# Performance work log

Hardware: AMD Instinct MI355X
Metric: run time of the kernel (lower is better)

The kernel has to match this reference:

```python
import jax, jax.numpy as jnp
import numpy as np

B, S, D, H = 1, 2048, 768, 12
WIN = 128            # window_size
HALF = WIN // 2      # 64
WN = WIN + 1         # each position attends to [i-64, i+64] inclusive -> 129 keys
DH = D // H


def setup_inputs() -> dict:
    key = jax.random.key(0)
    ks = jax.random.split(key, 8)
    scale = 0.02
    return {
        "query": jax.random.normal(ks[0], (B, S, D), dtype=jnp.float32),
        "key":   jax.random.normal(ks[1], (B, S, D), dtype=jnp.float32),
        "value": jax.random.normal(ks[2], (B, S, D), dtype=jnp.float32),
        "Wq": jax.random.normal(ks[3], (D, D), dtype=jnp.float32) * scale,
        "bq": jnp.zeros((D,), dtype=jnp.float32),
        "Wk": jax.random.normal(ks[4], (D, D), dtype=jnp.float32) * scale,
        "bk": jnp.zeros((D,), dtype=jnp.float32),
        "Wv": jax.random.normal(ks[5], (D, D), dtype=jnp.float32) * scale,
        "bv": jnp.zeros((D,), dtype=jnp.float32),
        "Wo": jax.random.normal(ks[6], (D, D), dtype=jnp.float32) * scale,
        "bo": jnp.zeros((D,), dtype=jnp.float32),
    }


def reference(query, key, value, Wq, bq, Wk, bk, Wv, bv, Wo, bo):
    b, s, d = query.shape
    # Linear projections, split heads: [B,S,H,DH]
    q = (query @ Wq + bq).reshape(b, s, H, DH)
    k = (key   @ Wk + bk).reshape(b, s, H, DH)
    v = (value @ Wv + bv).reshape(b, s, H, DH)

    # Window gather indices: pos[i, j] = i - HALF + j, j in [0, WN)
    pos = jnp.arange(s)[:, None] + (jnp.arange(WN)[None, :] - HALF)  # [S, WN]
    valid = (pos >= 0) & (pos < s)                                   # [S, WN]
    idx = jnp.clip(pos, 0, s - 1)

    kw = k[:, idx]  # [B, S, WN, H, DH]
    vw = v[:, idx]  # [B, S, WN, H, DH]

    scores = jnp.einsum('bshd,bswhd->bhsw', q, kw) / np.sqrt(DH)     # [B,H,S,WN]
    scores = jnp.where(valid[None, None, :, :], scores, -jnp.inf)
    attn = jax.nn.softmax(scores, axis=-1)

    ctx = jnp.einsum('bhsw,bswhd->bshd', attn, vw).reshape(b, s, d)  # [B,S,D]
    return ctx @ Wo + bo
```

## Files before the change

### kernel.cpp

```cpp
#include <hip/hip_runtime.h>
#include <math.h>

#define S_LEN 2048
#define DM 768
#define NHEAD 12
#define DHEAD 64
#define HALF_W 64

typedef _Float16 half8 __attribute__((ext_vector_type(8)));
typedef _Float16 half4_t __attribute__((ext_vector_type(4)));
typedef float floatx4 __attribute__((ext_vector_type(4)));

typedef const __attribute__((address_space(1))) unsigned int* gas_ptr;
typedef __attribute__((address_space(3))) unsigned int* las_ptr;
__device__ __forceinline__ void gld_lds16(const void* g, void* l) {
  __builtin_amdgcn_global_load_lds((gas_ptr)g, (las_ptr)l, 16, 0, 0);
}

__global__ __launch_bounds__(256)
void prep_w_kernel(const float* __restrict__ Wq, const float* __restrict__ Wk,
                   const float* __restrict__ Wv, const float* __restrict__ Wo,
                   _Float16* __restrict__ Tq, _Float16* __restrict__ Tk,
                   _Float16* __restrict__ Tv, _Float16* __restrict__ To) {
  __shared__ float t[64][65];
  int b = blockIdx.x;
  int z = b / 144, rem = b % 144;
  const float* W = z == 0 ? Wq : z == 1 ? Wk : z == 2 ? Wv : Wo;
  _Float16* T = z == 0 ? Tq : z == 1 ? Tk : z == 2 ? Tv : To;
  int n0 = (rem % 12) * 64, k0 = (rem / 12) * 64;
  int tx = threadIdx.x & 15, ty = threadIdx.x >> 4;
#pragma unroll
  for (int i = 0; i < 4; ++i) {
    int row = ty + i * 16;
    float4 v = *(const float4*)(W + (size_t)(k0 + row) * DM + n0 + tx * 4);
    t[row][tx * 4 + 0] = v.x; t[row][tx * 4 + 1] = v.y;
    t[row][tx * 4 + 2] = v.z; t[row][tx * 4 + 3] = v.w;
  }
  __syncthreads();
#pragma unroll
  for (int i = 0; i < 4; ++i) {
    int nn = ty + i * 16, kk = tx * 4;
    half4_t h = {(_Float16)t[kk + 0][nn], (_Float16)t[kk + 1][nn],
                 (_Float16)t[kk + 2][nn], (_Float16)t[kk + 3][nn]};
    *(half4_t*)(T + (size_t)(n0 + nn) * DM + k0 + kk) = h;
  }
}

#define GBM 64
#define GBN 128
#define GBK 64
#define ACH 17

__global__ __launch_bounds__(256, 4)
void gemm_qkv_kernel(const float* __restrict__ A0, const float* __restrict__ A1,
                     const float* __restrict__ A2, const _Float16* __restrict__ W0,
                     const _Float16* __restrict__ W1, const _Float16* __restrict__ W2,
                     const float* __restrict__ b0, const float* __restrict__ b1,
                     const float* __restrict__ b2, _Float16* __restrict__ Q,
                     _Float16* __restrict__ K, _Float16* __restrict__ Vt) {
  __shared__ __align__(16) float Asf[GBM * ACH * 4];
  __shared__ __align__(16) _Float16 Bs[GBN * GBK];
  const int bid = blockIdx.x;
  const int xcd = bid & 7;
  const int li = bid >> 3;
  const int panel = xcd * 12 + li / 6;
  const int nb = li % 6;
  const int z = panel >> 5;
  const int m0 = (panel & 31) * GBM;
  const int n0 = nb * GBN;
  const float* A = z == 0 ? A0 : z == 1 ? A1 : A2;
  const _Float16* Wt = z == 0 ? W0 : z == 1 ? W1 : W2;
  const float* bias = z == 0 ? b0 : z == 1 ? b1 : b2;

  const int tid = threadIdx.x;
  const int lane = tid & 63;
  const int w = tid >> 6;
  const int lr = lane & 15;
  const int lq = lane >> 4;
  const int wm = w >> 1, wn = w & 1;
  const int wb = tid & 192;

  floatx4 acc[2][4] = {};

  for (int k0 = 0; k0 < DM; k0 += GBK) {
    __syncthreads();
#pragma unroll
    for (int i = 0; i < 5; ++i) {
      if (i < 4 || tid < 64) {
        int s = i * 256 + tid;
        int m = s / ACH, pos = s % ACH;
        int ch = pos < 16 ? pos : 15;
        gld_lds16(A + (size_t)(m0 + m) * DM + k0 + ch * 4, &Asf[(i * 256 + wb) * 4]);
      }
    }
#pragma unroll
    for (int i = 0; i < 4; ++i) {
      int c = i * 256 + tid;
      int n = c >> 3, j = c & 7, jg = j ^ (n & 7);
      gld_lds16(Wt + (size_t)(n0 + n) * DM + k0 + jg * 8, &Bs[(i * 256 + wb) * 8]);
    }
    __syncthreads();

#pragma unroll
    for (int kh = 0; kh < 2; ++kh) {
      half8 af[2], bf[4];
#pragma unroll
      for (int mt = 0; mt < 2; ++mt) {
        int m = wm * 32 + mt * 16 + lr;
        int j0 = kh * 8 + lq * 2;
        float4 f0 = *(const float4*)&Asf[(m * ACH + j0) * 4];
        float4 f1 = *(const float4*)&Asf[(m * ACH + j0 + 1) * 4];
        af[mt] = half8{(_Float16)f0.x, (_Float16)f0.y, (_Float16)f0.z, (_Float16)f0.w,
                       (_Float16)f1.x, (_Float16)f1.y, (_Float16)f1.z, (_Float16)f1.w};
      }
#pragma unroll
      for (int nt = 0; nt < 4; ++nt) {
        int n = wn * 64 + nt * 16 + lr;
        int j = (kh * 4 + lq) ^ (n & 7);
        bf[nt] = *(const half8*)&Bs[n * GBK + j * 8];
      }
#pragma unroll
      for (int mt = 0; mt < 2; ++mt)
#pragma unroll
        for (int nt = 0; nt < 4; ++nt)
          acc[mt][nt] = __builtin_amdgcn_mfma_f32_16x16x32_f16(af[mt], bf[nt], acc[mt][nt], 0, 0, 0);
    }
  }

#pragma unroll
  for (int mt = 0; mt < 2; ++mt) {
    int row0 = m0 + wm * 32 + mt * 16 + lq * 4;
#pragma unroll
    for (int nt = 0; nt < 4; ++nt) {
      int col = n0 + wn * 64 + nt * 16 + lr;
      float bv = bias[col];
      if (z == 2) {
        half4_t o = {(_Float16)(acc[mt][nt][0] + bv), (_Float16)(acc[mt][nt][1] + bv),
                     (_Float16)(acc[mt][nt][2] + bv), (_Float16)(acc[mt][nt][3] + bv)};
        *(half4_t*)(Vt + (size_t)col * S_LEN + row0) = o;
      } else {
        _Float16* H = z == 0 ? Q : K;
#pragma unroll
        for (int rr = 0; rr < 4; ++rr)
          H[(size_t)(row0 + rr) * DM + col] = (_Float16)(acc[mt][nt][rr] + bv);
      }
    }
  }
}

#define OBM 64
#define OBN 64

__global__ __launch_bounds__(256, 6)
void gemm_out_kernel(const _Float16* __restrict__ A, const _Float16* __restrict__ Wt,
                     const float* __restrict__ bias, float* __restrict__ C) {
  __shared__ __align__(16) _Float16 As[OBM * GBK];
  __shared__ __align__(16) _Float16 Bs[OBN * GBK];
  const int bid = blockIdx.x;
  const int xcd = bid & 7;
  const int li = bid >> 3;
  const int m0 = (xcd * 4 + li / 12) * OBM;
  const int n0 = (li % 12) * OBN;
  const int tid = threadIdx.x;
  const int lane = tid & 63;
  const int w = tid >> 6;
  const int lr = lane & 15;
  const int lq = lane >> 4;
  const int wm = w >> 1, wn = w & 1;
  const int wb = tid & 192;

  floatx4 acc[2][2] = {};

  for (int k0 = 0; k0 < DM; k0 += GBK) {
    __syncthreads();
#pragma unroll
    for (int i = 0; i < 2; ++i) {
      int c = i * 256 + tid;
      int m = c >> 3, j = c & 7, jg = j ^ (m & 7);
      gld_lds16(A + (size_t)(m0 + m) * DM + k0 + jg * 8, &As[(i * 256 + wb) * 8]);
    }
#pragma unroll
    for (int i = 0; i < 2; ++i) {
      int c = i * 256 + tid;
      int n = c >> 3, j = c & 7, jg = j ^ (n & 7);
      gld_lds16(Wt + (size_t)(n0 + n) * DM + k0 + jg * 8, &Bs[(i * 256 + wb) * 8]);
    }
    __syncthreads();

#pragma unroll
    for (int kh = 0; kh < 2; ++kh) {
      half8 af[2], bf[2];
#pragma unroll
      for (int mt = 0; mt < 2; ++mt) {
        int m = wm * 32 + mt * 16 + lr;
        int j = (kh * 4 + lq) ^ (m & 7);
        af[mt] = *(const half8*)&As[m * GBK + j * 8];
      }
#pragma unroll
      for (int nt = 0; nt < 2; ++nt) {
        int n = wn * 32 + nt * 16 + lr;
        int j = (kh * 4 + lq) ^ (n & 7);
        bf[nt] = *(const half8*)&Bs[n * GBK + j * 8];
      }
#pragma unroll
      for (int mt = 0; mt < 2; ++mt)
#pragma unroll
        for (int nt = 0; nt < 2; ++nt)
          acc[mt][nt] = __builtin_amdgcn_mfma_f32_16x16x32_f16(af[mt], bf[nt], acc[mt][nt], 0, 0, 0);
    }
  }

#pragma unroll
  for (int mt = 0; mt < 2; ++mt) {
    int row0 = m0 + wm * 32 + mt * 16 + lq * 4;
#pragma unroll
    for (int nt = 0; nt < 2; ++nt) {
      int col = n0 + wn * 32 + nt * 16 + lr;
      float bv = bias[col];
#pragma unroll
      for (int rr = 0; rr < 4; ++rr)
        C[(size_t)(row0 + rr) * DM + col] = acc[mt][nt][rr] + bv;
    }
  }
}

#define ATQ 32

__global__ __launch_bounds__(256, 3)
void swattn_mfma_kernel(const _Float16* __restrict__ qh, const _Float16* __restrict__ kh,
                        const _Float16* __restrict__ vt, _Float16* __restrict__ ctx) {
  __shared__ __align__(16) _Float16 Ks[160 * 64];
  __shared__ __align__(16) _Float16 Vs[64 * 168];
  __shared__ __align__(16) _Float16 QP[32 * 168];
  __shared__ float red[4][32];

  const int tid = threadIdx.x;
  const int lane = tid & 63, w = tid >> 6;
  const int lr = lane & 15, lq = lane >> 4;
  const int bid = blockIdx.x;
  const int x = bid & 7, mid = (bid >> 3) & 7, h = bid >> 6;
  const int s0 = (x * 8 + mid) * ATQ;
  const int wb = tid & 192;

  {
    int r = tid >> 3, j = tid & 7, jg = j ^ (r & 7);
    gld_lds16(qh + (size_t)(s0 + r) * DM + h * DHEAD + jg * 8, &QP[wb * 8]);
  }
#pragma unroll
  for (int i = 0; i < 5; ++i) {
    int c = i * 256 + tid;
    int r = c >> 3, j = c & 7, jg = j ^ (r & 7);
    int pos = s0 - HALF_W + r;
    pos = pos < 0 ? 0 : (pos > S_LEN - 1 ? S_LEN - 1 : pos);
    gld_lds16(kh + (size_t)pos * DM + h * DHEAD + jg * 8, &Ks[(i * 256 + wb) * 8]);
  }
#pragma unroll
  for (int i = 0; i < 6; ++i) {
    int c = i * 256 + tid;
    if (c < 1344) {
      int r = c / 21, j = c % 21;
      int cb = s0 - HALF_W + j * 8;
      cb = cb < 0 ? 0 : (cb > S_LEN - 8 ? S_LEN - 8 : cb);
      gld_lds16(vt + (size_t)(h * DHEAD + r) * S_LEN + cb, &Vs[(i * 256 + wb) * 8]);
    }
  }
  __syncthreads();

  const int qt = w & 1, ph = w >> 1;
  floatx4 sc[5];
  {
    half8 aq[2];
#pragma unroll
    for (int k2 = 0; k2 < 2; ++k2) {
      int r = qt * 16 + lr, j = (k2 * 4 + lq) ^ (r & 7);
      aq[k2] = *(const half8*)&QP[r * DHEAD + j * 8];
    }
#pragma unroll
    for (int t = 0; t < 5; ++t) {
      int pt = ph * 5 + t;
      floatx4 a = {};
#pragma unroll
      for (int k2 = 0; k2 < 2; ++k2) {
        int r = pt * 16 + lr, j = (k2 * 4 + lq) ^ (r & 7);
        half8 bk = *(const half8*)&Ks[r * DHEAD + j * 8];
        a = __builtin_amdgcn_mfma_f32_16x16x32_f16(aq[k2], bk, a, 0, 0, 0);
      }
      sc[t] = a;
    }
  }

  const int qbase = qt * 16 + lq * 4;
  float m4[4] = {-1e30f, -1e30f, -1e30f, -1e30f};
#pragma unroll
  for (int t = 0; t < 5; ++t) {
    int p = (ph * 5 + t) * 16 + lr;
    int g = s0 - HALF_W + p;
#pragma unroll
    for (int rr = 0; rr < 4; ++rr) {
      int q = qbase + rr;
      bool ok = (p >= q) && (p <= q + 128) && (g >= 0) && (g < S_LEN);
      float v = ok ? sc[t][rr] * 0.125f : -1e30f;
      sc[t][rr] = v;
      m4[rr] = fmaxf(m4[rr], v);
    }
  }
#pragma unroll
  for (int off = 1; off <= 8; off <<= 1)
#pragma unroll
    for (int rr = 0; rr < 4; ++rr) m4[rr] = fmaxf(m4[rr], __shfl_xor(m4[rr], off, 64));
  if (lr == 0)
#pragma unroll
    for (int rr = 0; rr < 4; ++rr) red[ph][qbase + rr] = m4[rr];
  __syncthreads();

  float ss[4] = {0.f, 0.f, 0.f, 0.f};
  float mm[4];
#pragma unroll
  for (int rr = 0; rr < 4; ++rr)
    mm[rr] = fmaxf(red[0][qbase + rr], red[1][qbase + rr]);
#pragma unroll
  for (int t = 0; t < 5; ++t)
#pragma unroll
    for (int rr = 0; rr < 4; ++rr) {
      float e = __expf(sc[t][rr] - mm[rr]);
      sc[t][rr] = e;
      ss[rr] += e;
    }
#pragma unroll
  for (int off = 1; off <= 8; off <<= 1)
#pragma unroll
    for (int rr = 0; rr < 4; ++rr) ss[rr] += __shfl_xor(ss[rr], off, 64);
  if (lr == 0)
#pragma unroll
    for (int rr = 0; rr < 4; ++rr) red[2 + ph][qbase + rr] = ss[rr];
  __syncthreads();

#pragma unroll
  for (int rr = 0; rr < 4; ++rr) {
    float inv = 1.f / (red[2][qbase + rr] + red[3][qbase + rr]);
#pragma unroll
    for (int t = 0; t < 5; ++t) {
      int p = (ph * 5 + t) * 16 + lr;
      QP[(qbase + rr) * 168 + p] = (_Float16)(sc[t][rr] * inv);
    }
  }
  __syncthreads();

  {
    const int qt2 = w & 1;
    const int dt0 = (w >> 1) * 2;
    floatx4 a0 = {}, a1 = {};
#pragma unroll
    for (int ks = 0; ks < 5; ++ks) {
      half8 ap = *(const half8*)&QP[(qt2 * 16 + lr) * 168 + ks * 32 + lq * 8];
      half8 bv0 = *(const half8*)&Vs[(dt0 * 16 + lr) * 168 + ks * 32 + lq * 8];
      half8 bv1 = *(const half8*)&Vs[((dt0 + 1) * 16 + lr) * 168 + ks * 32 + lq * 8];
      a0 = __builtin_amdgcn_mfma_f32_16x16x32_f16(ap, bv0, a0, 0, 0, 0);
      a1 = __builtin_amdgcn_mfma_f32_16x16x32_f16(ap, bv1, a1, 0, 0, 0);
    }
#pragma unroll
    for (int rr = 0; rr < 4; ++rr) {
      size_t row = (size_t)(s0 + qt2 * 16 + lq * 4 + rr) * DM + h * DHEAD;
      ctx[row + dt0 * 16 + lr] = (_Float16)a0[rr];
      ctx[row + (dt0 + 1) * 16 + lr] = (_Float16)a1[rr];
    }
  }
}

extern "C" void kernel_launch(void* const* d_in, const int* in_sizes, int n_in,
                              void* d_out, int out_size, void* d_ws, size_t ws_size,
                              hipStream_t stream) {
  const float* query = (const float*)d_in[0];
  const float* key   = (const float*)d_in[1];
  const float* value = (const float*)d_in[2];
  const float* Wq = (const float*)d_in[3];
  const float* bq = (const float*)d_in[4];
  const float* Wk = (const float*)d_in[5];
  const float* bk = (const float*)d_in[6];
  const float* Wv = (const float*)d_in[7];
  const float* bv = (const float*)d_in[8];
  const float* Wo = (const float*)d_in[9];
  const float* bo = (const float*)d_in[10];
  float* out = (float*)d_out;

  const size_t nel = (size_t)S_LEN * DM;
  const size_t wel = (size_t)DM * DM;
  _Float16* Wtq = (_Float16*)d_ws;
  _Float16* Wtk = Wtq + wel;
  _Float16* Wtv = Wtk + wel;
  _Float16* Wto = Wtv + wel;
  _Float16* qh = Wto + wel;
  _Float16* khb = qh + nel;
  _Float16* Vtg = khb + nel;
  _Float16* ctxh = Vtg + nel;

  prep_w_kernel<<<dim3(576), 256, 0, stream>>>(Wq, Wk, Wv, Wo, Wtq, Wtk, Wtv, Wto);
  gemm_qkv_kernel<<<dim3(576), 256, 0, stream>>>(
      query, key, value, Wtq, Wtk, Wtv, bq, bk, bv, qh, khb, Vtg);
  swattn_mfma_kernel<<<dim3((S_LEN / ATQ) * NHEAD), 256, 0, stream>>>(qh, khb, Vtg, ctxh);
  gemm_out_kernel<<<dim3(384), 256, 0, stream>>>(ctxh, Wto, bo, out);
}
```

Baseline: 130.1 us.

## Pre-convert QKV activations to fp16 in prep kernel and simplify GEMM A tiles

The prep kernel now also converts the query/key/value activations from fp32 to fp16 into workspace buffers, so the QKV GEMM loads fp16 A tiles with an XOR-swizzled layout and does no per-fragment conversion. LDS use for A is halved, which allows raising the occupancy hint in launch bounds from 4 to 6. The cost is an extra full read and write pass over the activations in the prep kernel. The ctx buffer reuses the now-dead Aq workspace region.

```diff
diff --git a/kernel.cpp b/kernel.cpp
--- a/kernel.cpp
+++ b/kernel.cpp
@@ -18,47 +18,60 @@
 }
 
 __global__ __launch_bounds__(256)
-void prep_w_kernel(const float* __restrict__ Wq, const float* __restrict__ Wk,
-                   const float* __restrict__ Wv, const float* __restrict__ Wo,
-                   _Float16* __restrict__ Tq, _Float16* __restrict__ Tk,
-                   _Float16* __restrict__ Tv, _Float16* __restrict__ To) {
+void prep_kernel(const float* __restrict__ Wq, const float* __restrict__ Wk,
+                 const float* __restrict__ Wv, const float* __restrict__ Wo,
+                 _Float16* __restrict__ Tq, _Float16* __restrict__ Tk,
+                 _Float16* __restrict__ Tv, _Float16* __restrict__ To,
+                 const float* __restrict__ qs, const float* __restrict__ ks,
+                 const float* __restrict__ vs, _Float16* __restrict__ Aq,
+                 _Float16* __restrict__ Ak, _Float16* __restrict__ Av) {
   __shared__ float t[64][65];
   int b = blockIdx.x;
-  int z = b / 144, rem = b % 144;
-  const float* W = z == 0 ? Wq : z == 1 ? Wk : z == 2 ? Wv : Wo;
-  _Float16* T = z == 0 ? Tq : z == 1 ? Tk : z == 2 ? Tv : To;
-  int n0 = (rem % 12) * 64, k0 = (rem / 12) * 64;
-  int tx = threadIdx.x & 15, ty = threadIdx.x >> 4;
-#pragma unroll
-  for (int i = 0; i < 4; ++i) {
-    int row = ty + i * 16;
-    float4 v = *(const float4*)(W + (size_t)(k0 + row) * DM + n0 + tx * 4);
-    t[row][tx * 4 + 0] = v.x; t[row][tx * 4 + 1] = v.y;
-    t[row][tx * 4 + 2] = v.z; t[row][tx * 4 + 3] = v.w;
-  }
-  __syncthreads();
-#pragma unroll
-  for (int i = 0; i < 4; ++i) {
-    int nn = ty + i * 16, kk = tx * 4;
-    half4_t h = {(_Float16)t[kk + 0][nn], (_Float16)t[kk + 1][nn],
-                 (_Float16)t[kk + 2][nn], (_Float16)t[kk + 3][nn]};
-    *(half4_t*)(T + (size_t)(n0 + nn) * DM + k0 + kk) = h;
+  if (b < 576) {
+    int z = b / 144, rem = b % 144;
+    const float* W = z == 0 ? Wq : z == 1 ? Wk : z == 2 ? Wv : Wo;
+    _Float16* T = z == 0 ? Tq : z == 1 ? Tk : z == 2 ? Tv : To;
+    int n0 = (rem % 12) * 64, k0 = (rem / 12) * 64;
+    int tx = threadIdx.x & 15, ty = threadIdx.x >> 4;
+#pragma unroll
+    for (int i = 0; i < 4; ++i) {
+      int row = ty + i * 16;
+      float4 v = *(const float4*)(W + (size_t)(k0 + row) * DM + n0 + tx * 4);
+      t[row][tx * 4 + 0] = v.x; t[row][tx * 4 + 1] = v.y;
+      t[row][tx * 4 + 2] = v.z; t[row][tx * 4 + 3] = v.w;
+    }
+    __syncthreads();
+#pragma unroll
+    for (int i = 0; i < 4; ++i) {
+      int nn = ty + i * 16, kk = tx * 4;
+      half4_t h = {(_Float16)t[kk + 0][nn], (_Float16)t[kk + 1][nn],
+                   (_Float16)t[kk + 2][nn], (_Float16)t[kk + 3][nn]};
+      *(half4_t*)(T + (size_t)(n0 + nn) * DM + k0 + kk) = h;
+    }
+  } else {
+    int i = b - 576;
+    int z = i / 1536;
+    const float* s = z == 0 ? qs : z == 1 ? ks : vs;
+    _Float16* d = z == 0 ? Aq : z == 1 ? Ak : Av;
+    int idx = (i % 1536) * 256 + threadIdx.x;
+    float4 v = ((const float4*)s)[idx];
+    half4_t h = {(_Float16)v.x, (_Float16)v.y, (_Float16)v.z, (_Float16)v.w};
+    ((half4_t*)d)[idx] = h;
   }
 }
 
 #define GBM 64
 #define GBN 128
 #define GBK 64
-#define ACH 17
-
-__global__ __launch_bounds__(256, 4)
-void gemm_qkv_kernel(const float* __restrict__ A0, const float* __restrict__ A1,
-                     const float* __restrict__ A2, const _Float16* __restrict__ W0,
+
+__global__ __launch_bounds__(256, 6)
+void gemm_qkv_kernel(const _Float16* __restrict__ A0, const _Float16* __restrict__ A1,
+                     const _Float16* __restrict__ A2, const _Float16* __restrict__ W0,
                      const _Float16* __restrict__ W1, const _Float16* __restrict__ W2,
                      const float* __restrict__ b0, const float* __restrict__ b1,
                      const float* __restrict__ b2, _Float16* __restrict__ Q,
                      _Float16* __restrict__ K, _Float16* __restrict__ Vt) {
-  __shared__ __align__(16) float Asf[GBM * ACH * 4];
+  __shared__ __align__(16) _Float16 As[GBM * GBK];
   __shared__ __align__(16) _Float16 Bs[GBN * GBK];
   const int bid = blockIdx.x;
   const int xcd = bid & 7;
@@ -68,7 +81,7 @@
   const int z = panel >> 5;
   const int m0 = (panel & 31) * GBM;
   const int n0 = nb * GBN;
-  const float* A = z == 0 ? A0 : z == 1 ? A1 : A2;
+  const _Float16* A = z == 0 ? A0 : z == 1 ? A1 : A2;
   const _Float16* Wt = z == 0 ? W0 : z == 1 ? W1 : W2;
   const float* bias = z == 0 ? b0 : z == 1 ? b1 : b2;
 
@@ -85,13 +98,10 @@
   for (int k0 = 0; k0 < DM; k0 += GBK) {
     __syncthreads();
 #pragma unroll
-    for (int i = 0; i < 5; ++i) {
-      if (i < 4 || tid < 64) {
-        int s = i * 256 + tid;
-        int m = s / ACH, pos = s % ACH;
-        int ch = pos < 16 ? pos : 15;
-        gld_lds16(A + (size_t)(m0 + m) * DM + k0 + ch * 4, &Asf[(i * 256 + wb) * 4]);
-      }
+    for (int i = 0; i < 2; ++i) {
+      int c = i * 256 + tid;
+      int m = c >> 3, j = c & 7, jg = j ^ (m & 7);
+      gld_lds16(A + (size_t)(m0 + m) * DM + k0 + jg * 8, &As[(i * 256 + wb) * 8]);
     }
 #pragma unroll
     for (int i = 0; i < 4; ++i) {
@@ -107,11 +117,8 @@
 #pragma unroll
       for (int mt = 0; mt < 2; ++mt) {
         int m = wm * 32 + mt * 16 + lr;
-        int j0 = kh * 8 + lq * 2;
-        float4 f0 = *(const float4*)&Asf[(m * ACH + j0) * 4];
-        float4 f1 = *(const float4*)&Asf[(m * ACH + j0 + 1) * 4];
-        af[mt] = half8{(_Float16)f0.x, (_Float16)f0.y, (_Float16)f0.z, (_Float16)f0.w,
-                       (_Float16)f1.x, (_Float16)f1.y, (_Float16)f1.z, (_Float16)f1.w};
+        int j = (kh * 4 + lq) ^ (m & 7);
+        af[mt] = *(const half8*)&As[m * GBK + j * 8];
       }
 #pragma unroll
       for (int nt = 0; nt < 4; ++nt) {
@@ -385,18 +392,22 @@
 
   const size_t nel = (size_t)S_LEN * DM;
   const size_t wel = (size_t)DM * DM;
-  _Float16* Wtq = (_Float16*)d_ws;
+  _Float16* Aq = (_Float16*)d_ws;
+  _Float16* Ak = Aq + nel;
+  _Float16* Av = Ak + nel;
+  _Float16* Wtq = Av + nel;
   _Float16* Wtk = Wtq + wel;
   _Float16* Wtv = Wtk + wel;
   _Float16* Wto = Wtv + wel;
   _Float16* qh = Wto + wel;
   _Float16* khb = qh + nel;
   _Float16* Vtg = khb + nel;
-  _Float16* ctxh = Vtg + nel;
-
-  prep_w_kernel<<<dim3(576), 256, 0, stream>>>(Wq, Wk, Wv, Wo, Wtq, Wtk, Wtv, Wto);
+  _Float16* ctxh = Aq;
+
+  prep_kernel<<<dim3(576 + 4608), 256, 0, stream>>>(
+      Wq, Wk, Wv, Wo, Wtq, Wtk, Wtv, Wto, query, key, value, Aq, Ak, Av);
   gemm_qkv_kernel<<<dim3(576), 256, 0, stream>>>(
-      query, key, value, Wtq, Wtk, Wtv, bq, bk, bv, qh, khb, Vtg);
+      Aq, Ak, Av, Wtq, Wtk, Wtv, bq, bk, bv, qh, khb, Vtg);
   swattn_mfma_kernel<<<dim3((S_LEN / ATQ) * NHEAD), 256, 0, stream>>>(qh, khb, Vtg, ctxh);
   gemm_out_kernel<<<dim3(384), 256, 0, stream>>>(ctxh, Wto, bo, out);
 }
```

Measured after the change: 133.2 us. +2.4%, slower.
